# Kernel optimization log

Measured on AMD Instinct MI355X. Metric: run time of the kernel, lower is better.

The kernel has to match this reference:

```python
import jax, jax.numpy as jnp
import numpy as np

B, T, V, C, K = 256, 2048, 128, 512, 10


def setup_inputs() -> dict:
    key = jax.random.key(0)
    k0, k1, k2, k3 = jax.random.split(key, 4)
    x = jax.random.normal(k0, (B, C), dtype=jnp.float32)
    # kappa_old: running attention position, non-negative, somewhere in [0, T)
    kappa_old = jax.random.uniform(k1, (B, K), dtype=jnp.float32) * T
    # onehots: one-hot encoded text, (B, T, V)
    char_ids = jax.random.randint(k2, (B, T), 0, V)
    onehots = jax.nn.one_hot(char_ids, V, dtype=jnp.float32)
    # Linear(cell_size, 3*K) params; torch stores weight as (out, in)
    W = jax.random.normal(k3, (3 * K, C), dtype=jnp.float32) * 0.02
    b = jnp.zeros((3 * K,), dtype=jnp.float32)
    return {"x": x, "kappa_old": kappa_old, "onehots": onehots, "W": W, "b": b}


def reference(x, kappa_old, onehots, W, b):
    max_text_len = onehots.shape[1]
    params = jnp.exp(x @ W.T + b)                      # (B, 3K)
    alpha, beta, pre_kappa = jnp.split(params, 3, axis=-1)  # each (B, K)
    kappa = kappa_old + pre_kappa                      # (B, K)
    indices = jnp.arange(max_text_len, dtype=x.dtype)  # (T,)
    # gravity: (B, K, T) via broadcast, then exp + alpha-weighted reduce over K
    gravity = -beta[:, :, None] * (kappa[:, :, None] - indices) ** 2
    phi = jnp.einsum("bk,bkt->bt", alpha, jnp.exp(gravity))  # (B, T)
    w = jnp.einsum("bt,btv->bv", phi, onehots)               # (B, V)
    return (w, kappa, phi)
```

## Files before the change

### kernel.cpp

```cpp
#include <hip/hip_runtime.h>

#define B_ 256
#define T_ 2048
#define V_ 128
#define C_ 512
#define K_ 10

#define W_OFF 0
#define KAPPA_OFF (B_ * V_)
#define PHI_OFF   (B_ * V_ + B_ * K_)

#define S_ 8
#define TS_ (T_ / S_)
#define RPT 32
#define EPS 1e-7f

typedef float f4_t __attribute__((ext_vector_type(4)));

__global__ __launch_bounds__(256) void window_fused(
    const float* __restrict__ x, const float* __restrict__ kappa_old,
    const float* __restrict__ W, const float* __restrict__ bias,
    const float* __restrict__ onehots, float* __restrict__ out) {
  const int s = blockIdx.x;
  const int b = blockIdx.y;
  const int tid = threadIdx.x;

  __shared__ f4_t xs4[C_ / 4];
  __shared__ float alpha_s[K_];
  __shared__ float beta_s[K_];
  __shared__ float kap_s[K_];
  __shared__ float phs[TS_];

  if (tid < C_ / 4) xs4[tid] = ((const f4_t*)(x + b * C_))[tid];
  __syncthreads();

  const int j = tid >> 3;
  const int l = tid & 7;
  if (j < 3 * K_) {
    const f4_t* Wr = (const f4_t*)(W + j * C_);
    f4_t a4 = {0.f, 0.f, 0.f, 0.f};
#pragma unroll
    for (int m = 0; m < 16; ++m) a4 += Wr[m * 8 + l] * xs4[m * 8 + l];
    float acc = (a4.x + a4.y) + (a4.z + a4.w);
    acc += __shfl_down(acc, 4, 8);
    acc += __shfl_down(acc, 2, 8);
    acc += __shfl_down(acc, 1, 8);
    if (l == 0) {
      const float p = __expf(acc + bias[j]);
      if (j < K_) {
        alpha_s[j] = p;
      } else if (j < 2 * K_) {
        beta_s[j - K_] = p;
      } else {
        const int k = j - 2 * K_;
        const float kk = kappa_old[b * K_ + k] + p;
        kap_s[k] = kk;
        if (s == 0) out[KAPPA_OFF + b * K_ + k] = kk;
      }
    }
  }
  __syncthreads();

  {
    const int t = s * TS_ + tid;
    const float ft = (float)t;
    float ph = 0.0f;
#pragma unroll
    for (int k = 0; k < K_; k++) {
      const float d = kap_s[k] - ft;
      ph += alpha_s[k] * __expf(-beta_s[k] * d * d);
    }
    phs[tid] = ph;
    out[PHI_OFF + b * T_ + t] = ph;
  }
  __syncthreads();

  const int vg = tid & 31;
  const int tr = tid >> 5;
  const f4_t* p0 = (const f4_t*)(onehots +
                   ((size_t)b * T_ + (size_t)s * TS_ + tr) * V_) + vg;

  unsigned mask = 0;
#pragma unroll
  for (int jj = 0; jj < RPT; ++jj)
    if (phs[tr + 8 * jj] >= EPS) mask |= 1u << jj;

  f4_t acc = {0.f, 0.f, 0.f, 0.f};
  int j0 = -1, j1 = -1, j2 = -1, j3 = -1;
  f4_t o0 = acc, o1 = acc, o2 = acc, o3 = acc;
  if (mask) { j0 = __builtin_ctz(mask); mask &= mask - 1;
              o0 = __builtin_nontemporal_load(p0 + j0 * 256); }
  if (mask) { j1 = __builtin_ctz(mask); mask &= mask - 1;
              o1 = __builtin_nontemporal_load(p0 + j1 * 256); }
  if (mask) { j2 = __builtin_ctz(mask); mask &= mask - 1;
              o2 = __builtin_nontemporal_load(p0 + j2 * 256); }
  if (mask) { j3 = __builtin_ctz(mask); mask &= mask - 1;
              o3 = __builtin_nontemporal_load(p0 + j3 * 256); }
  while (j0 >= 0) {
    acc += phs[tr + 8 * j0] * o0;
    j0 = j1; o0 = o1;
    j1 = j2; o1 = o2;
    j2 = j3; o2 = o3;
    if (mask) { j3 = __builtin_ctz(mask); mask &= mask - 1;
                o3 = __builtin_nontemporal_load(p0 + j3 * 256); }
    else j3 = -1;
  }

  __shared__ float red[8 * V_];
  *(f4_t*)&red[tr * V_ + vg * 4] = acc;
  __syncthreads();

  if (tid < V_) {
    float s0 = 0.0f;
#pragma unroll
    for (int r = 0; r < 8; r++) s0 += red[r * V_ + tid];
    atomicAdd(&out[W_OFF + b * V_ + tid], s0);
  }
}

extern "C" void kernel_launch(void* const* d_in, const int* in_sizes, int n_in,
                              void* d_out, int out_size, void* d_ws,
                              size_t ws_size, hipStream_t stream) {
  const float* x         = (const float*)d_in[0];
  const float* kappa_old = (const float*)d_in[1];
  const float* onehots   = (const float*)d_in[2];
  const float* W         = (const float*)d_in[3];
  const float* bias      = (const float*)d_in[4];
  float* out = (float*)d_out;

  hipMemsetAsync(d_out, 0, B_ * V_ * sizeof(float), stream);
  window_fused<<<dim3(S_, B_), dim3(256), 0, stream>>>(x, kappa_old, W, bias,
                                                       onehots, out);
}
```

Before: 309.1 us.

## Use one 1024-thread block per batch row, dropping atomics and memset

Replaces the 8-way T split (8 blocks of 256 threads per batch) with a single 1024-thread block per batch row. The linear projection is computed once per row instead of eight times, the final w reduction writes directly without atomicAdd, and the separate memset launch is removed. The trade-off is a smaller grid (256 blocks) of larger blocks, with more shared memory per block, which may reduce occupancy and latency hiding for the sparse onehot gathers.

```diff
diff --git a/kernel.cpp b/kernel.cpp
--- a/kernel.cpp
+++ b/kernel.cpp
@@ -10,41 +10,43 @@
 #define KAPPA_OFF (B_ * V_)
 #define PHI_OFF   (B_ * V_ + B_ * K_)
 
-#define S_ 8
-#define TS_ (T_ / S_)
-#define RPT 32
 #define EPS 1e-7f
+
+#define NG 32
+#define RPG (T_ / NG)
 
 typedef float f4_t __attribute__((ext_vector_type(4)));
 
-__global__ __launch_bounds__(256) void window_fused(
+__global__ __launch_bounds__(1024) void window_fused(
     const float* __restrict__ x, const float* __restrict__ kappa_old,
     const float* __restrict__ W, const float* __restrict__ bias,
     const float* __restrict__ onehots, float* __restrict__ out) {
-  const int s = blockIdx.x;
-  const int b = blockIdx.y;
+  const int b = blockIdx.x;
   const int tid = threadIdx.x;
 
   __shared__ f4_t xs4[C_ / 4];
   __shared__ float alpha_s[K_];
   __shared__ float beta_s[K_];
   __shared__ float kap_s[K_];
-  __shared__ float phs[TS_];
+  __shared__ float phs[T_];
+  __shared__ float red[NG * V_];
 
   if (tid < C_ / 4) xs4[tid] = ((const f4_t*)(x + b * C_))[tid];
   __syncthreads();
 
-  const int j = tid >> 3;
-  const int l = tid & 7;
+  const int j = tid >> 5;
+  const int l = tid & 31;
   if (j < 3 * K_) {
     const f4_t* Wr = (const f4_t*)(W + j * C_);
     f4_t a4 = {0.f, 0.f, 0.f, 0.f};
 #pragma unroll
-    for (int m = 0; m < 16; ++m) a4 += Wr[m * 8 + l] * xs4[m * 8 + l];
+    for (int m = 0; m < 4; ++m) a4 += Wr[m * 32 + l] * xs4[m * 32 + l];
     float acc = (a4.x + a4.y) + (a4.z + a4.w);
-    acc += __shfl_down(acc, 4, 8);
-    acc += __shfl_down(acc, 2, 8);
-    acc += __shfl_down(acc, 1, 8);
+    acc += __shfl_down(acc, 16, 32);
+    acc += __shfl_down(acc, 8, 32);
+    acc += __shfl_down(acc, 4, 32);
+    acc += __shfl_down(acc, 2, 32);
+    acc += __shfl_down(acc, 1, 32);
     if (l == 0) {
       const float p = __expf(acc + bias[j]);
       if (j < K_) {
@@ -55,14 +57,15 @@
         const int k = j - 2 * K_;
         const float kk = kappa_old[b * K_ + k] + p;
         kap_s[k] = kk;
-        if (s == 0) out[KAPPA_OFF + b * K_ + k] = kk;
+        out[KAPPA_OFF + b * K_ + k] = kk;
       }
     }
   }
   __syncthreads();
 
-  {
-    const int t = s * TS_ + tid;
+#pragma unroll
+  for (int half = 0; half < 2; ++half) {
+    const int t = tid + half * 1024;
     const float ft = (float)t;
     float ph = 0.0f;
 #pragma unroll
@@ -70,51 +73,50 @@
       const float d = kap_s[k] - ft;
       ph += alpha_s[k] * __expf(-beta_s[k] * d * d);
     }
-    phs[tid] = ph;
+    phs[t] = ph;
     out[PHI_OFF + b * T_ + t] = ph;
   }
   __syncthreads();
 
+  const int g = tid >> 5;
   const int vg = tid & 31;
-  const int tr = tid >> 5;
-  const f4_t* p0 = (const f4_t*)(onehots +
-                   ((size_t)b * T_ + (size_t)s * TS_ + tr) * V_) + vg;
+  const f4_t* p0 =
+      (const f4_t*)(onehots + ((size_t)b * T_ + g) * V_) + vg;
 
-  unsigned mask = 0;
-#pragma unroll
-  for (int jj = 0; jj < RPT; ++jj)
-    if (phs[tr + 8 * jj] >= EPS) mask |= 1u << jj;
+  unsigned long long mask = 0;
+#pragma unroll 8
+  for (int jj = 0; jj < RPG; ++jj)
+    if (phs[g + 32 * jj] >= EPS) mask |= 1ull << jj;
 
   f4_t acc = {0.f, 0.f, 0.f, 0.f};
   int j0 = -1, j1 = -1, j2 = -1, j3 = -1;
   f4_t o0 = acc, o1 = acc, o2 = acc, o3 = acc;
-  if (mask) { j0 = __builtin_ctz(mask); mask &= mask - 1;
-              o0 = __builtin_nontemporal_load(p0 + j0 * 256); }
-  if (mask) { j1 = __builtin_ctz(mask); mask &= mask - 1;
-              o1 = __builtin_nontemporal_load(p0 + j1 * 256); }
-  if (mask) { j2 = __builtin_ctz(mask); mask &= mask - 1;
-              o2 = __builtin_nontemporal_load(p0 + j2 * 256); }
-  if (mask) { j3 = __builtin_ctz(mask); mask &= mask - 1;
-              o3 = __builtin_nontemporal_load(p0 + j3 * 256); }
+  if (mask) { j0 = __builtin_ctzll(mask); mask &= mask - 1;
+              o0 = __builtin_nontemporal_load(p0 + (size_t)j0 * 1024); }
+  if (mask) { j1 = __builtin_ctzll(mask); mask &= mask - 1;
+              o1 = __builtin_nontemporal_load(p0 + (size_t)j1 * 1024); }
+  if (mask) { j2 = __builtin_ctzll(mask); mask &= mask - 1;
+              o2 = __builtin_nontemporal_load(p0 + (size_t)j2 * 1024); }
+  if (mask) { j3 = __builtin_ctzll(mask); mask &= mask - 1;
+              o3 = __builtin_nontemporal_load(p0 + (size_t)j3 * 1024); }
   while (j0 >= 0) {
-    acc += phs[tr + 8 * j0] * o0;
+    acc += phs[g + 32 * j0] * o0;
     j0 = j1; o0 = o1;
     j1 = j2; o1 = o2;
     j2 = j3; o2 = o3;
-    if (mask) { j3 = __builtin_ctz(mask); mask &= mask - 1;
-                o3 = __builtin_nontemporal_load(p0 + j3 * 256); }
+    if (mask) { j3 = __builtin_ctzll(mask); mask &= mask - 1;
+                o3 = __builtin_nontemporal_load(p0 + (size_t)j3 * 1024); }
     else j3 = -1;
   }
 
-  __shared__ float red[8 * V_];
-  *(f4_t*)&red[tr * V_ + vg * 4] = acc;
+  *(f4_t*)&red[g * V_ + vg * 4] = acc;
   __syncthreads();
 
   if (tid < V_) {
     float s0 = 0.0f;
 #pragma unroll
-    for (int r = 0; r < 8; r++) s0 += red[r * V_ + tid];
-    atomicAdd(&out[W_OFF + b * V_ + tid], s0);
+    for (int r = 0; r < NG; r++) s0 += red[r * V_ + tid];
+    out[W_OFF + b * V_ + tid] = s0;
   }
 }
 
@@ -128,7 +130,6 @@
   const float* bias      = (const float*)d_in[4];
   float* out = (float*)d_out;
 
-  hipMemsetAsync(d_out, 0, B_ * V_ * sizeof(float), stream);
-  window_fused<<<dim3(S_, B_), dim3(256), 0, stream>>>(x, kappa_old, W, bias,
-                                                       onehots, out);
+  window_fused<<<dim3(B_), dim3(1024), 0, stream>>>(x, kappa_old, W, bias,
+                                                    onehots, out);
 }
```

Result: no change. 307.9 us (-0.4%).
